# Kernel optimization log

Hardware: AMD Instinct MI355X
Metric: run time of the kernel (lower is better)

## Reference

```python
import jax, jax.numpy as jnp
import numpy as np

E = 256      # embedding_dim
H = 8        # num_heads
D = E // H   # head_dim = 32
F = 1024     # dim_feedforward
EPS = 1e-5


def layer_norm(x, gamma, beta):
    mu = jnp.mean(x, axis=-1, keepdims=True)
    var = jnp.var(x, axis=-1, keepdims=True)
    return (x - mu) * jax.lax.rsqrt(var + EPS) * gamma + beta


def setup_inputs() -> dict:
    key = jax.random.key(0)
    ks = jax.random.split(key, 12)
    s = lambda fan_in: 1.0 / np.sqrt(fan_in)
    src = jax.random.normal(ks[0], (4, 2048, E), dtype=jnp.float32)
    w_in = jax.random.uniform(ks[1], (3 * E, E), minval=-s(E), maxval=s(E), dtype=jnp.float32)
    w_out = jax.random.uniform(ks[2], (E, E), minval=-s(E), maxval=s(E), dtype=jnp.float32)
    w1 = jax.random.uniform(ks[3], (F, E), minval=-s(E), maxval=s(E), dtype=jnp.float32)
    b1 = jax.random.uniform(ks[4], (F,), minval=-s(E), maxval=s(E), dtype=jnp.float32)
    w2 = jax.random.uniform(ks[5], (E, F), minval=-s(F), maxval=s(F), dtype=jnp.float32)
    b2 = jax.random.uniform(ks[6], (E,), minval=-s(F), maxval=s(F), dtype=jnp.float32)
    g1 = jnp.ones((E,), jnp.float32)
    beta1 = jnp.zeros((E,), jnp.float32)
    g2 = jnp.ones((E,), jnp.float32)
    beta2 = jnp.zeros((E,), jnp.float32)
    return {"src": src, "w_in": w_in, "w_out": w_out, "w1": w1, "b1": b1,
            "w2": w2, "b2": b2, "g1": g1, "beta1": beta1, "g2": g2, "beta2": beta2}


def reference(src, w_in, w_out, w1, b1, w2, b2, g1, beta1, g2, beta2):
    B, S, _ = src.shape
    scale = D ** (-0.5)
    # --- pre-norm self-attention block ---
    x = layer_norm(src, g1, beta1)                 # [B,S,E]
    qkv = x @ w_in.T                               # [B,S,3E]
    q, k, v = jnp.split(qkv, 3, axis=-1)
    q = q.reshape(B, S, H, D).transpose(0, 2, 1, 3)  # [B,H,S,D]
    k = k.reshape(B, S, H, D).transpose(0, 2, 1, 3)
    v = v.reshape(B, S, H, D).transpose(0, 2, 1, 3)
    scores = jnp.einsum('bhqd,bhkd->bhqk', q, k) * scale  # [B,H,S,S]
    attn = jax.nn.softmax(scores, axis=-1)
    out = jnp.einsum('bhqk,bhkd->bhqd', attn, v)   # [B,H,S,D]
    out = out.transpose(0, 2, 1, 3).reshape(B, S, E)
    src = src + out @ w_out.T
    # --- pre-norm FFN block ---
    y = layer_norm(src, g2, beta2)
    y = jax.nn.relu(y @ w1.T + b1) @ w2.T + b2
    return src + y
```

## Files before the change

kernel.cpp:

```cpp
#include <hip/hip_runtime.h>
#include <hip/hip_bf16.h>
#include <math.h>

typedef unsigned short u16;
typedef unsigned int   u32;
using bf16x8 = __attribute__((ext_vector_type(8))) short;
using f32x4  = __attribute__((ext_vector_type(4))) float;
using f32x16 = __attribute__((ext_vector_type(16))) float;
using u32v4  = __attribute__((ext_vector_type(4))) u32;

#define TE 256
#define TH 8
#define TS 2048
#define TB 4
#define NTOK 8192
#define QSCALE 0.2550120651552454f
#define EXP2(x) __builtin_amdgcn_exp2f(x)

__device__ __forceinline__ void async16(const u16* g, u16* l) {
    __builtin_amdgcn_global_load_lds(
        (const __attribute__((address_space(1))) u32*)g,
        (__attribute__((address_space(3))) u32*)l, 16, 0, 0);
}
__device__ __forceinline__ u32 pkbf(float a, float b) {
    u32 ua = __float_as_uint(a) + 0x8000u;
    u32 ub = __float_as_uint(b) + 0x8000u;
    return __builtin_amdgcn_perm(ub, ua, 0x07060302u);
}
__device__ __forceinline__ u16 bf1(float a) {
    return (u16)((__float_as_uint(a) + 0x8000u) >> 16);
}

__global__ __launch_bounds__(256) void ln_bf(const float* __restrict__ in,
        u16* __restrict__ out, const float* __restrict__ gamma,
        const float* __restrict__ beta) {
    int row  = blockIdx.x * 4 + (threadIdx.x >> 6);
    int lane = threadIdx.x & 63;
    float4 v = ((const float4*)(in + (size_t)row * TE))[lane];
    float s  = v.x + v.y + v.z + v.w;
    float s2 = v.x*v.x + v.y*v.y + v.z*v.z + v.w*v.w;
    #pragma unroll
    for (int off = 32; off > 0; off >>= 1) {
        s  += __shfl_down(s,  off, 64);
        s2 += __shfl_down(s2, off, 64);
    }
    s  = __shfl(s,  0, 64);
    s2 = __shfl(s2, 0, 64);
    float mu = s * (1.f / TE);
    float rs = rsqrtf(s2 * (1.f / TE) - mu * mu + 1e-5f);
    float4 g = ((const float4*)gamma)[lane];
    float4 b = ((const float4*)beta )[lane];
    u32 lo = pkbf((v.x - mu) * rs * g.x + b.x, (v.y - mu) * rs * g.y + b.y);
    u32 hi = pkbf((v.z - mu) * rs * g.z + b.z, (v.w - mu) * rs * g.w + b.w);
    ((uint2*)(out + (size_t)row * TE))[lane] = make_uint2(lo, hi);
}

__global__ __launch_bounds__(256) void convw(const float* __restrict__ s0, u16* d0,
        const float* __restrict__ s1, u16* d1, const float* __restrict__ s2, u16* d2,
        const float* __restrict__ s3, u16* d3) {
    int i = (blockIdx.x * 256 + threadIdx.x) * 4;
    const float* s; u16* d;
    if      (i < 196608) { s = s0; d = d0; }
    else if (i < 262144) { s = s1; d = d1; i -= 196608; }
    else if (i < 524288) { s = s2; d = d2; i -= 262144; }
    else                 { s = s3; d = d3; i -= 524288; }
    float4 v = *(const float4*)(s + i);
    *(uint2*)(d + i) = make_uint2(pkbf(v.x, v.y), pkbf(v.z, v.w));
}

template<int K, int BM, int EPI>
__global__ __launch_bounds__(256) void mgemm(const u16* __restrict__ A,
        const u16* __restrict__ W, const float* __restrict__ bias,
        const float* __restrict__ R, float* __restrict__ Cf,
        u16* __restrict__ Cb, int M) {
    constexpr int BN = BM;
    __shared__ u16 Al[2][BM * 32];
    __shared__ u16 Wl[2][BN * 32];
    const int tid = threadIdx.x, w = tid >> 6, l = tid & 63;
    const int n0 = blockIdx.y * BM;
    const int m0 = blockIdx.x * BN;
    constexpr int NT = (BM == 128) ? 4 : 2;
    constexpr int NF = (BM == 128) ? 4 : 2;
    const int tw = (w & 1) * NT * 16;
    const int fw = (w >> 1) * NF * 16;
    const int fr = l & 15, fq = l >> 4;
    const int sr = l >> 2, sc = (l & 3) * 8;
    f32x4 acc[NT][NF];
    #pragma unroll
    for (int t = 0; t < NT; t++)
        #pragma unroll
        for (int f = 0; f < NF; f++)
            #pragma unroll
            for (int r = 0; r < 4; r++) acc[t][f][r] = 0.f;

    for (int k0 = 0; k0 < K; k0 += 64) {
        __syncthreads();
        #pragma unroll
        for (int hh = 0; hh < 2; hh++) {
            const int kc = k0 + hh * 32;
            if (BM == 128) {
                #pragma unroll
                for (int c = 0; c < 2; c++) {
                    int rr = (w * 2 + c) * 16 + sr;
                    async16(A + (size_t)(n0 + rr) * K + kc + sc, &Al[hh][(w * 2 + c) * 512]);
                    async16(W + (size_t)(m0 + rr) * K + kc + sc, &Wl[hh][(w * 2 + c) * 512]);
                }
            } else {
                int rr = w * 16 + sr;
                async16(A + (size_t)(n0 + rr) * K + kc + sc, &Al[hh][w * 512]);
                async16(W + (size_t)(m0 + rr) * K + kc + sc, &Wl[hh][w * 512]);
            }
        }
        __syncthreads();
        #pragma unroll
        for (int hh = 0; hh < 2; hh++) {
            bf16x8 af[NT], wf[NF];
            #pragma unroll
            for (int t = 0; t < NT; t++)
                af[t] = *(const bf16x8*)&Al[hh][(tw + t * 16 + fr) * 32 + fq * 8];
            #pragma unroll
            for (int f = 0; f < NF; f++)
                wf[f] = *(const bf16x8*)&Wl[hh][(fw + f * 16 + fr) * 32 + fq * 8];
            #pragma unroll
            for (int t = 0; t < NT; t++)
                #pragma unroll
                for (int f = 0; f < NF; f++)
                    acc[t][f] = __builtin_amdgcn_mfma_f32_16x16x32_bf16(
                        wf[f], af[t], acc[t][f], 0, 0, 0);
        }
    }
    #pragma unroll
    for (int t = 0; t < NT; t++) {
        const int tok = n0 + tw + t * 16 + fr;
        #pragma unroll
        for (int f = 0; f < NF; f++) {
            const int fb = m0 + fw + f * 16 + fq * 4;
            f32x4 v = acc[t][f];
            if (EPI == 0) {
                if (fb < 512) {
                    const float qs = (fb < 256) ? QSCALE : 1.f;
                    *(uint2*)(Cb + (size_t)tok * 512 + fb) =
                        make_uint2(pkbf(v[0]*qs, v[1]*qs), pkbf(v[2]*qs, v[3]*qs));
                } else {
                    const int hh = (fb - 512) >> 5, dd = (fb - 512) & 31;
                    u16* vt = (u16*)Cf +
                        ((size_t)((tok >> 11) * 8 + hh) * 32 + dd) * 2048 + (tok & 2047);
                    vt[0]    = bf1(v[0]);
                    vt[2048] = bf1(v[1]);
                    vt[4096] = bf1(v[2]);
                    vt[6144] = bf1(v[3]);
                }
            } else if (EPI == 1) {
                float4 r4 = *(const float4*)(R + (size_t)tok * M + fb);
                *(float4*)(Cf + (size_t)tok * M + fb) =
                    make_float4(v[0]+r4.x, v[1]+r4.y, v[2]+r4.z, v[3]+r4.w);
            } else if (EPI == 2) {
                float4 b4 = *(const float4*)(bias + fb);
                *(uint2*)(Cb + (size_t)tok * M + fb) = make_uint2(
                    pkbf(fmaxf(v[0]+b4.x, 0.f), fmaxf(v[1]+b4.y, 0.f)),
                    pkbf(fmaxf(v[2]+b4.z, 0.f), fmaxf(v[3]+b4.w, 0.f)));
            } else {
                float4 b4 = *(const float4*)(bias + fb);
                float4 r4 = *(const float4*)(R + (size_t)tok * M + fb);
                *(float4*)(Cf + (size_t)tok * M + fb) = make_float4(
                    v[0]+b4.x+r4.x, v[1]+b4.y+r4.y, v[2]+b4.z+r4.z, v[3]+b4.w+r4.w);
            }
        }
    }
}

__global__ __launch_bounds__(256, 4) void attn_k(const u16* __restrict__ qk,
        const u16* __restrict__ vt, u16* __restrict__ attn) {
    const int id = blockIdx.x;
    const int bh   = (id & 7) * 4 + (id >> 8);
    const int tile = (id >> 3) & 31;
    const int b = bh >> 3, h = bh & 7;
    const int tid = threadIdx.x, w = tid >> 6, l = tid & 63;
    const int qw = w & 1, kw = w >> 1;
    const int lq = l & 31, hi = l >> 5;
    const size_t btok = (size_t)b * TS;
    const int q0 = tile * 64 + qw * 32;

    __shared__ float mrg[2304];

    const u16* qrow = qk + (btok + q0 + lq) * 512 + h * 32 + hi * 8;
    bf16x8 qf0 = *(const bf16x8*)qrow;
    bf16x8 qf1 = *(const bf16x8*)(qrow + 16);

    const u16* kb = qk + (btok + (size_t)kw * 1024) * 512 + 256 + h * 32 + hi * 8;
    const u16* vb = vt + ((size_t)bh * 32 + lq) * 2048 + kw * 1024 + hi * 8;

    f32x16 zf, o;
    #pragma unroll
    for (int r = 0; r < 16; r++) { zf[r] = 0.f; o[r] = 0.f; }
    float ps = 0.f;

    u32 koff = (u32)lq * 512;
    u32 voff = 0;
    for (int it = 0; it < 32; ++it) {
        bf16x8 kf0 = *(const bf16x8*)(kb + koff);
        bf16x8 kf1 = *(const bf16x8*)(kb + koff + 16);
        bf16x8 vf0 = *(const bf16x8*)(vb + voff);
        bf16x8 vf1 = *(const bf16x8*)(vb + voff + 16);
        koff += 32 * 512;
        voff += 32;
        f32x16 p = __builtin_amdgcn_mfma_f32_32x32x16_bf16(kf0, qf0, zf, 0, 0, 0);
        p = __builtin_amdgcn_mfma_f32_32x32x16_bf16(kf1, qf1, p, 0, 0, 0);
        float e[16];
        #pragma unroll
        for (int r = 0; r < 16; r++) e[r] = EXP2(p[r]);
        ps += ((e[0]+e[1]) + (e[2]+e[3])) + ((e[4]+e[5]) + (e[6]+e[7]))
            + ((e[8]+e[9]) + (e[10]+e[11])) + ((e[12]+e[13]) + (e[14]+e[15]));
        u32 a[8];
        #pragma unroll
        for (int j = 0; j < 8; j++)
            asm("v_cvt_pk_bf16_f32 %0, %1, %2"
                : "=v"(a[j]) : "v"(e[2*j]), "v"(e[2*j+1]));
        asm("v_permlane32_swap_b32 %0, %1" : "+v"(a[0]), "+v"(a[2]));
        asm("v_permlane32_swap_b32 %0, %1" : "+v"(a[1]), "+v"(a[3]));
        asm("v_permlane32_swap_b32 %0, %1" : "+v"(a[4]), "+v"(a[6]));
        asm("v_permlane32_swap_b32 %0, %1" : "+v"(a[5]), "+v"(a[7]));
        u32v4 t0 = {a[0], a[1], a[2], a[3]};
        u32v4 t1 = {a[4], a[5], a[6], a[7]};
        bf16x8 pf0 = __builtin_bit_cast(bf16x8, t0);
        bf16x8 pf1 = __builtin_bit_cast(bf16x8, t1);
        o = __builtin_amdgcn_mfma_f32_32x32x16_bf16(vf0, pf0, o, 0, 0, 0);
        o = __builtin_amdgcn_mfma_f32_32x32x16_bf16(vf1, pf1, o, 0, 0, 0);
    }
    ps += __shfl_xor(ps, 32, 64);

    if (kw == 1) {
        float* d = mrg + (qw * 64 + l) * 18;
        #pragma unroll
        for (int r = 0; r < 16; r++) d[r] = o[r];
        d[16] = ps;
    }
    __syncthreads();
    if (kw == 0) {
        const float* d = mrg + (qw * 64 + l) * 18;
        #pragma unroll
        for (int r = 0; r < 16; r++) o[r] += d[r];
        ps += d[16];
        float inv = 1.f / ps;
        int tok = (int)btok + q0 + lq;
        u16* orow = attn + (size_t)tok * 256 + h * 32 + hi * 4;
        #pragma unroll
        for (int g = 0; g < 4; g++)
            *(uint2*)(orow + g * 8) = make_uint2(
                pkbf(o[4*g]*inv, o[4*g+1]*inv), pkbf(o[4*g+2]*inv, o[4*g+3]*inv));
    }
}

extern "C" void kernel_launch(void* const* d_in, const int* in_sizes, int n_in,
                              void* d_out, int out_size, void* d_ws, size_t ws_size,
                              hipStream_t stream) {
    const float* src  = (const float*)d_in[0];
    const float* w_in = (const float*)d_in[1];
    const float* w_out= (const float*)d_in[2];
    const float* w1   = (const float*)d_in[3];
    const float* b1   = (const float*)d_in[4];
    const float* w2   = (const float*)d_in[5];
    const float* b2   = (const float*)d_in[6];
    const float* g1   = (const float*)d_in[7];
    const float* be1  = (const float*)d_in[8];
    const float* g2   = (const float*)d_in[9];
    const float* be2  = (const float*)d_in[10];
    float* out = (float*)d_out;

    u16* xb    = (u16*)d_ws;
    u16* qkb   = xb + (size_t)NTOK * 256;
    u16* vtb   = qkb + (size_t)NTOK * 512;
    u16* attnb = xb;
    u16* h1b   = (u16*)d_ws;
    u16* x2b   = (u16*)((char*)d_ws + (size_t)NTOK * 1024 * 2);
    u16* wib   = x2b + (size_t)NTOK * 256;
    u16* wob   = wib + 768 * 256;
    u16* w1b   = wob + 256 * 256;
    u16* w2b   = w1b + 1024 * 256;

    convw<<<768, 256, 0, stream>>>(w_in, wib, w_out, wob, w1, w1b, w2, w2b);
    ln_bf<<<NTOK / 4, 256, 0, stream>>>(src, xb, g1, be1);
    mgemm<256, 128, 0><<<dim3(6, 64), 256, 0, stream>>>(
        xb, wib, nullptr, nullptr, (float*)vtb, qkb, 768);
    attn_k<<<dim3(1024), 256, 0, stream>>>(qkb, vtb, attnb);
    mgemm<256, 64, 1><<<dim3(4, 128), 256, 0, stream>>>(
        attnb, wob, nullptr, src, out, nullptr, 256);
    ln_bf<<<NTOK / 4, 256, 0, stream>>>(out, x2b, g2, be2);
    mgemm<256, 128, 2><<<dim3(8, 64), 256, 0, stream>>>(
        x2b, w1b, b1, nullptr, nullptr, h1b, 1024);
    mgemm<1024, 64, 3><<<dim3(4, 128), 256, 0, stream>>>(
        h1b, w2b, b2, out, out, nullptr, 256);
}
```

Baseline: 195.2 us.

## Store K/V in MFMA fragment order and prefetch next tile in attention

The QKV GEMM epilogue now writes K and V into per-head, per-32-key tile buffers laid out in the exact lane order the attention MFMA operands use. Each wave can then fetch its fragments as contiguous 16-byte-per-lane loads instead of strided row reads. The attention loop also register double-buffers the next tile's K/V fragments and unrolls by two to hide load latency behind the MFMAs. The cost is a more scattered store pattern in the GEMM epilogue and extra live registers in the attention kernel.

```diff
diff --git a/kernel.cpp b/kernel.cpp
--- a/kernel.cpp
+++ b/kernel.cpp
@@ -137,18 +137,29 @@
             const int fb = m0 + fw + f * 16 + fq * 4;
             f32x4 v = acc[t][f];
             if (EPI == 0) {
-                if (fb < 512) {
-                    const float qs = (fb < 256) ? QSCALE : 1.f;
-                    *(uint2*)(Cb + (size_t)tok * 512 + fb) =
-                        make_uint2(pkbf(v[0]*qs, v[1]*qs), pkbf(v[2]*qs, v[3]*qs));
+                if (fb < 256) {
+                    *(uint2*)(Cb + (size_t)tok * 256 + fb) = make_uint2(
+                        pkbf(v[0]*QSCALE, v[1]*QSCALE), pkbf(v[2]*QSCALE, v[3]*QSCALE));
+                } else if (fb < 512) {
+                    const int hh = (fb - 256) >> 5, dd = (fb - 256) & 31;
+                    const int bh = (tok >> 11) * 8 + hh;
+                    const int kv = tok & 2047, tile = kv >> 5, lq = kv & 31;
+                    const int fg = dd >> 4, hg = (dd >> 3) & 1, j = dd & 7;
+                    u16* kp = (u16*)bias +
+                        (((((size_t)bh * 64 + tile) * 2 + fg) * 2 + hg) * 32 + lq) * 8 + j;
+                    *(uint2*)kp = make_uint2(pkbf(v[0], v[1]), pkbf(v[2], v[3]));
                 } else {
                     const int hh = (fb - 512) >> 5, dd = (fb - 512) & 31;
-                    u16* vt = (u16*)Cf +
-                        ((size_t)((tok >> 11) * 8 + hh) * 32 + dd) * 2048 + (tok & 2047);
-                    vt[0]    = bf1(v[0]);
-                    vt[2048] = bf1(v[1]);
-                    vt[4096] = bf1(v[2]);
-                    vt[6144] = bf1(v[3]);
+                    const int bh = (tok >> 11) * 8 + hh;
+                    const int kv = tok & 2047, tile = kv >> 5, kvr = kv & 31;
+                    const int fg = kvr >> 4, hg = (kvr >> 3) & 1, j = kvr & 7;
+                    u16* vp = (u16*)R +
+                        ((((size_t)bh * 64 + tile) * 2 + fg) * 2 + hg) * 256 +
+                        (size_t)dd * 8 + j;
+                    vp[0]  = bf1(v[0]);
+                    vp[8]  = bf1(v[1]);
+                    vp[16] = bf1(v[2]);
+                    vp[24] = bf1(v[3]);
                 }
             } else if (EPI == 1) {
                 float4 r4 = *(const float4*)(R + (size_t)tok * M + fb);
@@ -169,8 +180,9 @@
     }
 }
 
-__global__ __launch_bounds__(256, 4) void attn_k(const u16* __restrict__ qk,
-        const u16* __restrict__ vt, u16* __restrict__ attn) {
+__global__ __launch_bounds__(256, 4) void attn_k(const u16* __restrict__ qb,
+        const u16* __restrict__ kfb, const u16* __restrict__ vfb,
+        u16* __restrict__ attn) {
     const int id = blockIdx.x;
     const int bh   = (id & 7) * 4 + (id >> 8);
     const int tile = (id >> 3) & 31;
@@ -183,29 +195,31 @@
 
     __shared__ float mrg[2304];
 
-    const u16* qrow = qk + (btok + q0 + lq) * 512 + h * 32 + hi * 8;
+    const u16* qrow = qb + (btok + q0 + lq) * 256 + h * 32 + hi * 8;
     bf16x8 qf0 = *(const bf16x8*)qrow;
     bf16x8 qf1 = *(const bf16x8*)(qrow + 16);
-
-    const u16* kb = qk + (btok + (size_t)kw * 1024) * 512 + 256 + h * 32 + hi * 8;
-    const u16* vb = vt + ((size_t)bh * 32 + lq) * 2048 + kw * 1024 + hi * 8;
 
     f32x16 zf, o;
     #pragma unroll
     for (int r = 0; r < 16; r++) { zf[r] = 0.f; o[r] = 0.f; }
     float ps = 0.f;
 
-    u32 koff = (u32)lq * 512;
-    u32 voff = 0;
+    const u16* kp = kfb + ((size_t)bh * 64 + kw * 32) * 1024 + l * 8;
+    const u16* vp = vfb + ((size_t)bh * 64 + kw * 32) * 1024 + l * 8;
+    bf16x8 k0 = *(const bf16x8*)kp;
+    bf16x8 k1 = *(const bf16x8*)(kp + 512);
+    bf16x8 v0 = *(const bf16x8*)vp;
+    bf16x8 v1 = *(const bf16x8*)(vp + 512);
+
+    #pragma unroll 2
     for (int it = 0; it < 32; ++it) {
-        bf16x8 kf0 = *(const bf16x8*)(kb + koff);
-        bf16x8 kf1 = *(const bf16x8*)(kb + koff + 16);
-        bf16x8 vf0 = *(const bf16x8*)(vb + voff);
-        bf16x8 vf1 = *(const bf16x8*)(vb + voff + 16);
-        koff += 32 * 512;
-        voff += 32;
-        f32x16 p = __builtin_amdgcn_mfma_f32_32x32x16_bf16(kf0, qf0, zf, 0, 0, 0);
-        p = __builtin_amdgcn_mfma_f32_32x32x16_bf16(kf1, qf1, p, 0, 0, 0);
+        kp += 1024; vp += 1024;
+        bf16x8 nk0 = *(const bf16x8*)kp;
+        bf16x8 nk1 = *(const bf16x8*)(kp + 512);
+        bf16x8 nv0 = *(const bf16x8*)vp;
+        bf16x8 nv1 = *(const bf16x8*)(vp + 512);
+        f32x16 p = __builtin_amdgcn_mfma_f32_32x32x16_bf16(k0, qf0, zf, 0, 0, 0);
+        p = __builtin_amdgcn_mfma_f32_32x32x16_bf16(k1, qf1, p, 0, 0, 0);
         float e[16];
         #pragma unroll
         for (int r = 0; r < 16; r++) e[r] = EXP2(p[r]);
@@ -224,8 +238,9 @@
         u32v4 t1 = {a[4], a[5], a[6], a[7]};
         bf16x8 pf0 = __builtin_bit_cast(bf16x8, t0);
         bf16x8 pf1 = __builtin_bit_cast(bf16x8, t1);
-        o = __builtin_amdgcn_mfma_f32_32x32x16_bf16(vf0, pf0, o, 0, 0, 0);
-        o = __builtin_amdgcn_mfma_f32_32x32x16_bf16(vf1, pf1, o, 0, 0, 0);
+        o = __builtin_amdgcn_mfma_f32_32x32x16_bf16(v0, pf0, o, 0, 0, 0);
+        o = __builtin_amdgcn_mfma_f32_32x32x16_bf16(v1, pf1, o, 0, 0, 0);
+        k0 = nk0; k1 = nk1; v0 = nv0; v1 = nv1;
     }
     ps += __shfl_xor(ps, 32, 64);
 
@@ -268,8 +283,9 @@
     float* out = (float*)d_out;
 
     u16* xb    = (u16*)d_ws;
-    u16* qkb   = xb + (size_t)NTOK * 256;
-    u16* vtb   = qkb + (size_t)NTOK * 512;
+    u16* qb    = xb + (size_t)NTOK * 256;
+    u16* kfbuf = qb + (size_t)NTOK * 256;
+    u16* vfbuf = kfbuf + (size_t)32 * 64 * 1024;
     u16* attnb = xb;
     u16* h1b   = (u16*)d_ws;
     u16* x2b   = (u16*)((char*)d_ws + (size_t)NTOK * 1024 * 2);
@@ -281,8 +297,8 @@
     convw<<<768, 256, 0, stream>>>(w_in, wib, w_out, wob, w1, w1b, w2, w2b);
     ln_bf<<<NTOK / 4, 256, 0, stream>>>(src, xb, g1, be1);
     mgemm<256, 128, 0><<<dim3(6, 64), 256, 0, stream>>>(
-        xb, wib, nullptr, nullptr, (float*)vtb, qkb, 768);
-    attn_k<<<dim3(1024), 256, 0, stream>>>(qkb, vtb, attnb);
+        xb, wib, (const float*)kfbuf, (const float*)vfbuf, nullptr, qb, 768);
+    attn_k<<<dim3(1024), 256, 0, stream>>>(qb, kfbuf, vfbuf, attnb);
     mgemm<256, 64, 1><<<dim3(4, 128), 256, 0, stream>>>(
         attnb, wob, nullptr, src, out, nullptr, 256);
     ln_bf<<<NTOK / 4, 256, 0, stream>>>(out, x2b, g2, be2);
```

After: 160.9 us. 17.6% less time.
